# Kernel tuning notes

Hardware: AMD Instinct MI355X
Metric: run time of the kernel (lower is better)

Reference implementation:

```python
import jax, jax.numpy as jnp
import numpy as np

C = 512
HSIZE = C // 4
D, H, W = 18, 24, 24
N = D * H * W


def setup_inputs() -> dict:
    key = jax.random.key(0)
    ks = jax.random.split(key, 6)
    features = jax.random.normal(ks[0], (1, C, D, H, W), dtype=jnp.float32)
    Wi = jax.random.normal(ks[1], (HSIZE, C), dtype=jnp.float32) * 0.02
    bi = jax.random.normal(ks[2], (HSIZE,), dtype=jnp.float32) * 0.02
    Wj = jax.random.normal(ks[3], (HSIZE, C), dtype=jnp.float32) * 0.02
    bj = jax.random.normal(ks[4], (HSIZE,), dtype=jnp.float32) * 0.02
    # attention_agregate: shape (head=1, 1), xavier-uniform in the original
    agg = jax.random.uniform(ks[5], (1, 1), dtype=jnp.float32, minval=-1.0, maxval=1.0)
    return {"features": features, "Wi": Wi, "bi": bi, "Wj": Wj, "bj": bj, "agg": agg}


def reference(features, Wi, bi, Wj, bj, agg):
    # features: [1, C, D, H, W]; 1x1x1 convs == channel-wise matmuls
    x = features.reshape(C, N)                      # [C, N]
    fi = (Wi @ x + bi[:, None]).T                   # [N, hsize]  (conv_i output, permuted)
    fj = Wj @ x + bj[:, None]                       # [hsize, N]  (conv_j output)
    fk = x.T                                        # [N, C]      (raw features, NOT conv_k)
    # original: attn = (fi @ fj) * agg / N ; out = attn @ fk
    # linear chain reassociated: fi @ (fj @ fk) * agg / N  (same math, no NxN intermediate)
    scale = agg[0, 0] / jnp.float32(N)
    out_flat = (fi @ (fj @ fk)) * scale             # [N, C]
    return features + out_flat.T.reshape(1, C, D, H, W)
```

## Files before the change

### kernel.cpp

```cpp
#include <hip/hip_runtime.h>
#include <hip/hip_bf16.h>

#define C_   512
#define HS   128
#define NN   10368

typedef __bf16 bf16x8 __attribute__((ext_vector_type(8)));
typedef __bf16 bf16x2 __attribute__((ext_vector_type(2)));
typedef float  f32x4  __attribute__((ext_vector_type(4)));

__device__ __forceinline__ bf16x8 load_f32x8_as_bf16(const float* __restrict__ p) {
    float4 v0 = *(const float4*)p;
    float4 v1 = *(const float4*)(p + 4);
    bf16x8 o;
    o[0] = (__bf16)v0.x; o[1] = (__bf16)v0.y; o[2] = (__bf16)v0.z; o[3] = (__bf16)v0.w;
    o[4] = (__bf16)v1.x; o[5] = (__bf16)v1.y; o[6] = (__bf16)v1.z; o[7] = (__bf16)v1.w;
    return o;
}

__global__ void k_fused12(const float* __restrict__ feat,
                          const float* __restrict__ Wi, const float* __restrict__ Wj,
                          const float* __restrict__ bi, const float* __restrict__ bj,
                          __bf16* __restrict__ xb, __bf16* __restrict__ fj,
                          __bf16* __restrict__ finm, float* __restrict__ Mtf) {
    const int b = blockIdx.x;
    const int t = threadIdx.x;
    if (b >= 324) {
        const int j = b - 324;
        f32x4 z = {0.f, 0.f, 0.f, 0.f};
        float* p = Mtf + j * 4096 + t * 16;
        *(f32x4*)(p) = z; *(f32x4*)(p + 4) = z;
        *(f32x4*)(p + 8) = z; *(f32x4*)(p + 12) = z;
        return;
    }
    __shared__ __bf16 xt[32][520];
    const int n0 = b * 32;
    {
        const int tn = t & 31;
        const int c2 = (t >> 5) * 2;
        for (int cc = 0; cc < 512; cc += 16) {
            const int c = cc + c2;
            float v0 = feat[(size_t)c * NN + n0 + tn];
            float v1 = feat[(size_t)(c + 1) * NN + n0 + tn];
            __bf16 b0 = (__bf16)v0, b1 = (__bf16)v1;
            xb[(size_t)c * NN + n0 + tn]       = b0;
            xb[(size_t)(c + 1) * NN + n0 + tn] = b1;
            bf16x2 pk; pk[0] = b0; pk[1] = b1;
            *(bf16x2*)&xt[tn][c] = pk;
        }
    }
    __syncthreads();
    const int w    = t >> 6;
    const int lane = t & 63;
    const int l16  = lane & 15;
    const int q    = lane >> 4;
    const int h0   = w * 32;
    f32x4 afj[2][2] = {};
    f32x4 afi[2][2] = {};
    for (int k = 0; k < 512; k += 32) {
        bf16x8 ln[2], wj[2], wi[2];
        #pragma unroll
        for (int i = 0; i < 2; i++)
            ln[i] = *(const bf16x8*)&xt[16 * i + l16][k + q * 8];
        #pragma unroll
        for (int i = 0; i < 2; i++)
            wj[i] = load_f32x8_as_bf16(Wj + (h0 + 16 * i + l16) * 512 + k + q * 8);
        #pragma unroll
        for (int i = 0; i < 2; i++)
            wi[i] = load_f32x8_as_bf16(Wi + (h0 + 16 * i + l16) * 512 + k + q * 8);
        #pragma unroll
        for (int i = 0; i < 2; i++)
            #pragma unroll
            for (int tt = 0; tt < 2; tt++) {
                afj[i][tt] = __builtin_amdgcn_mfma_f32_16x16x32_bf16(wj[i], ln[tt], afj[i][tt], 0, 0, 0);
                afi[i][tt] = __builtin_amdgcn_mfma_f32_16x16x32_bf16(ln[i], wi[tt], afi[i][tt], 0, 0, 0);
            }
    }
    #pragma unroll
    for (int i = 0; i < 2; i++)
        #pragma unroll
        for (int tt = 0; tt < 2; tt++)
            #pragma unroll
            for (int r = 0; r < 4; r++) {
                {
                    int h = h0 + 16 * i + q * 4 + r;
                    int n = n0 + 16 * tt + l16;
                    fj[(size_t)h * NN + n] = (__bf16)(afj[i][tt][r] + bj[h]);
                }
                {
                    int n = n0 + 16 * i + q * 4 + r;
                    int h = h0 + 16 * tt + l16;
                    finm[(size_t)n * HS + h] = (__bf16)(afi[i][tt][r] + bi[h]);
                }
            }
}

__global__ void k_gemm3(const __bf16* __restrict__ xb, const __bf16* __restrict__ fj,
                        float* __restrict__ Mtf) {
    __shared__ float red[4][64][17];
    const int b    = blockIdx.x;
    const int t    = threadIdx.x;
    const int v    = t >> 6;
    const int lane = t & 63;
    const int l16  = lane & 15;
    const int q    = lane >> 4;
    const int tile = b & 63, g = b >> 6;
    const int c0 = (tile >> 2) * 32, h0 = (tile & 3) * 32;
    const int chunk = g * 4 + v;
    const int s0 = (chunk * 324) >> 5;
    const int s1 = ((chunk + 1) * 324) >> 5;
    f32x4 acc[2][2] = {};
    for (int s = s0; s < s1; s++) {
        int k = s * 32;
        bf16x8 a[2], bb[2];
        #pragma unroll
        for (int i = 0; i < 2; i++)
            a[i] = *(const bf16x8*)(xb + (size_t)(c0 + 16 * i + l16) * NN + k + q * 8);
        #pragma unroll
        for (int tt = 0; tt < 2; tt++)
            bb[tt] = *(const bf16x8*)(fj + (size_t)(h0 + 16 * tt + l16) * NN + k + q * 8);
        #pragma unroll
        for (int i = 0; i < 2; i++)
            #pragma unroll
            for (int tt = 0; tt < 2; tt++)
                acc[i][tt] = __builtin_amdgcn_mfma_f32_16x16x32_bf16(a[i], bb[tt], acc[i][tt], 0, 0, 0);
    }
    #pragma unroll
    for (int i = 0; i < 2; i++)
        #pragma unroll
        for (int tt = 0; tt < 2; tt++)
            #pragma unroll
            for (int r = 0; r < 4; r++)
                red[v][lane][i * 8 + tt * 4 + r] = acc[i][tt][r];
    __syncthreads();
    #pragma unroll
    for (int u = 0; u < 4; u++) {
        const int idx = t * 4 + u;
        const int lane_e = idx >> 4, j = idx & 15;
        float s = red[0][lane_e][j] + red[1][lane_e][j]
                + red[2][lane_e][j] + red[3][lane_e][j];
        const int i = j >> 3, tt = (j >> 2) & 1, r = j & 3;
        const int qe = lane_e >> 4, le = lane_e & 15;
        const int c = c0 + 16 * i + qe * 4 + r;
        const int h = h0 + 16 * tt + le;
        atomicAdd(&Mtf[c * HS + h], s);
    }
}

__global__ void k_gemm4(const float* __restrict__ Mtf, const __bf16* __restrict__ finm,
                        const float* __restrict__ feat, const float* __restrict__ agg,
                        float* __restrict__ out) {
    const int w    = blockIdx.x * 4 + (threadIdx.x >> 6);
    const int lane = threadIdx.x & 63;
    const int l16  = lane & 15;
    const int q    = lane >> 4;
    const int c0 = (w & 15) * 32, n0 = (w >> 4) * 64;
    const float scale = agg[0] * (1.0f / (float)NN);
    f32x4 acc[2][4] = {};
    for (int k = 0; k < 128; k += 32) {
        bf16x8 a[2], b[4];
        #pragma unroll
        for (int i = 0; i < 2; i++)
            a[i] = load_f32x8_as_bf16(Mtf + (c0 + 16 * i + l16) * HS + k + q * 8);
        #pragma unroll
        for (int tt = 0; tt < 4; tt++)
            b[tt] = *(const bf16x8*)(finm + (size_t)(n0 + 16 * tt + l16) * HS + k + q * 8);
        #pragma unroll
        for (int i = 0; i < 2; i++)
            #pragma unroll
            for (int tt = 0; tt < 4; tt++)
                acc[i][tt] = __builtin_amdgcn_mfma_f32_16x16x32_bf16(a[i], b[tt], acc[i][tt], 0, 0, 0);
    }
    #pragma unroll
    for (int i = 0; i < 2; i++)
        #pragma unroll
        for (int tt = 0; tt < 4; tt++)
            #pragma unroll
            for (int r = 0; r < 4; r++) {
                int c = c0 + 16 * i + q * 4 + r;
                int n = n0 + 16 * tt + l16;
                size_t idx = (size_t)c * NN + n;
                out[idx] = feat[idx] + scale * acc[i][tt][r];
            }
}

extern "C" void kernel_launch(void* const* d_in, const int* in_sizes, int n_in,
                              void* d_out, int out_size, void* d_ws, size_t ws_size,
                              hipStream_t stream) {
    const float* feat = (const float*)d_in[0];
    const float* Wi   = (const float*)d_in[1];
    const float* bi   = (const float*)d_in[2];
    const float* Wj   = (const float*)d_in[3];
    const float* bj   = (const float*)d_in[4];
    const float* agg  = (const float*)d_in[5];
    float* out = (float*)d_out;

    char* ws = (char*)d_ws;
    __bf16* xb   = (__bf16*)(ws);
    __bf16* fj   = (__bf16*)(ws + 10616832);
    __bf16* finm = (__bf16*)(ws + 13271040);
    float*  Mtf  = (float*) (ws + 15925248);

    k_fused12<<<340, 256, 0, stream>>>(feat, Wi, Wj, bi, bj, xb, fj, finm, Mtf);
    k_gemm3<<<512, 256, 0, stream>>>(xb, fj, Mtf);
    k_gemm4<<<648, 256, 0, stream>>>(Mtf, finm, feat, agg, out);
}
```

Before: 137.5 us.

## Split fused projection into staging and GEMM kernels, raise grid parallelism

```diff
diff --git a/kernel.cpp b/kernel.cpp
--- a/kernel.cpp
+++ b/kernel.cpp
@@ -6,6 +6,7 @@
 #define NN   10368
 
 typedef __bf16 bf16x8 __attribute__((ext_vector_type(8)));
+typedef __bf16 bf16x4 __attribute__((ext_vector_type(4)));
 typedef __bf16 bf16x2 __attribute__((ext_vector_type(2)));
 typedef float  f32x4  __attribute__((ext_vector_type(4)));
 
@@ -18,86 +19,118 @@
     return o;
 }
 
-__global__ void k_fused12(const float* __restrict__ feat,
-                          const float* __restrict__ Wi, const float* __restrict__ Wj,
-                          const float* __restrict__ bi, const float* __restrict__ bj,
-                          __bf16* __restrict__ xb, __bf16* __restrict__ fj,
-                          __bf16* __restrict__ finm, float* __restrict__ Mtf) {
+__global__ void k_stage(const float* __restrict__ feat,
+                        const float* __restrict__ Wi, const float* __restrict__ Wj,
+                        __bf16* __restrict__ xb, __bf16* __restrict__ xt,
+                        __bf16* __restrict__ Wib, __bf16* __restrict__ Wjb,
+                        float* __restrict__ Mtf) {
     const int b = blockIdx.x;
     const int t = threadIdx.x;
-    if (b >= 324) {
-        const int j = b - 324;
-        f32x4 z = {0.f, 0.f, 0.f, 0.f};
-        float* p = Mtf + j * 4096 + t * 16;
-        *(f32x4*)(p) = z; *(f32x4*)(p + 4) = z;
-        *(f32x4*)(p + 8) = z; *(f32x4*)(p + 12) = z;
+    if (b >= 1296) {
+        const int j = b - 1296;
+        if (j < 4) {
+            const float* src = (j < 2) ? Wj : Wi;
+            __bf16* dst = (j < 2) ? Wjb : Wib;
+            const int off = (j & 1) * 32768;
+            #pragma unroll 4
+            for (int u = 0; u < 32; u++) {
+                const int idx = off + u * 1024 + t * 4;
+                float4 v = *(const float4*)(src + idx);
+                bf16x4 o;
+                o[0] = (__bf16)v.x; o[1] = (__bf16)v.y;
+                o[2] = (__bf16)v.z; o[3] = (__bf16)v.w;
+                *(bf16x4*)(dst + idx) = o;
+            }
+        } else {
+            const int z = j - 4;
+            f32x4 zv = {0.f, 0.f, 0.f, 0.f};
+            float* p = Mtf + z * 4096 + t * 16;
+            *(f32x4*)(p) = zv; *(f32x4*)(p + 4) = zv;
+            *(f32x4*)(p + 8) = zv; *(f32x4*)(p + 12) = zv;
+        }
         return;
     }
-    __shared__ __bf16 xt[32][520];
-    const int n0 = b * 32;
-    {
-        const int tn = t & 31;
-        const int c2 = (t >> 5) * 2;
-        for (int cc = 0; cc < 512; cc += 16) {
-            const int c = cc + c2;
-            float v0 = feat[(size_t)c * NN + n0 + tn];
-            float v1 = feat[(size_t)(c + 1) * NN + n0 + tn];
-            __bf16 b0 = (__bf16)v0, b1 = (__bf16)v1;
-            xb[(size_t)c * NN + n0 + tn]       = b0;
-            xb[(size_t)(c + 1) * NN + n0 + tn] = b1;
-            bf16x2 pk; pk[0] = b0; pk[1] = b1;
-            *(bf16x2*)&xt[tn][c] = pk;
+    __shared__ __bf16 ldt[64][66];
+    const int bn = b >> 3, bc = b & 7;
+    const int n0 = bn * 64, c0 = bc * 64;
+    const int i = t & 15;
+    const int g = t >> 4;
+    const int nl = 4 * i;
+    #pragma unroll
+    for (int p = 0; p < 2; p++) {
+        const int cl = 2 * g + 32 * p;
+        const float* s = feat + (size_t)(c0 + cl) * NN + n0 + nl;
+        float4 v0 = *(const float4*)s;
+        float4 v1 = *(const float4*)(s + NN);
+        bf16x4 o0, o1;
+        o0[0] = (__bf16)v0.x; o0[1] = (__bf16)v0.y; o0[2] = (__bf16)v0.z; o0[3] = (__bf16)v0.w;
+        o1[0] = (__bf16)v1.x; o1[1] = (__bf16)v1.y; o1[2] = (__bf16)v1.z; o1[3] = (__bf16)v1.w;
+        *(bf16x4*)(xb + (size_t)(c0 + cl) * NN + n0 + nl)     = o0;
+        *(bf16x4*)(xb + (size_t)(c0 + cl + 1) * NN + n0 + nl) = o1;
+        #pragma unroll
+        for (int jj = 0; jj < 4; jj++) {
+            bf16x2 pk; pk[0] = o0[jj]; pk[1] = o1[jj];
+            *(bf16x2*)&ldt[nl + jj][cl] = pk;
         }
     }
     __syncthreads();
-    const int w    = t >> 6;
+    #pragma unroll
+    for (int p = 0; p < 4; p++) {
+        const int nr = g + 16 * p;
+        const int cw = 4 * i;
+        bf16x2 a0 = *(const bf16x2*)&ldt[nr][cw];
+        bf16x2 a1 = *(const bf16x2*)&ldt[nr][cw + 2];
+        bf16x4 o; o[0] = a0[0]; o[1] = a0[1]; o[2] = a1[0]; o[3] = a1[1];
+        *(bf16x4*)(xt + (size_t)(n0 + nr) * C_ + c0 + cw) = o;
+    }
+}
+
+__global__ void k_gemm12(const __bf16* __restrict__ xt,
+                         const __bf16* __restrict__ Wjb, const __bf16* __restrict__ Wib,
+                         const float* __restrict__ bi, const float* __restrict__ bj,
+                         __bf16* __restrict__ fj, __bf16* __restrict__ finm) {
+    const int b = blockIdx.x;
+    const int t = threadIdx.x;
+    const int w = t >> 6;
     const int lane = t & 63;
-    const int l16  = lane & 15;
-    const int q    = lane >> 4;
-    const int h0   = w * 32;
-    f32x4 afj[2][2] = {};
-    f32x4 afi[2][2] = {};
+    const int l16 = lane & 15;
+    const int q   = lane >> 4;
+    const int n0 = (b >> 1) * 32;
+    const int h0 = (b & 1) * 64 + w * 16;
+    f32x4 afj[2] = {};
+    f32x4 afi[2] = {};
+    #pragma unroll 4
     for (int k = 0; k < 512; k += 32) {
-        bf16x8 ln[2], wj[2], wi[2];
-        #pragma unroll
-        for (int i = 0; i < 2; i++)
-            ln[i] = *(const bf16x8*)&xt[16 * i + l16][k + q * 8];
-        #pragma unroll
-        for (int i = 0; i < 2; i++)
-            wj[i] = load_f32x8_as_bf16(Wj + (h0 + 16 * i + l16) * 512 + k + q * 8);
-        #pragma unroll
-        for (int i = 0; i < 2; i++)
-            wi[i] = load_f32x8_as_bf16(Wi + (h0 + 16 * i + l16) * 512 + k + q * 8);
-        #pragma unroll
-        for (int i = 0; i < 2; i++)
-            #pragma unroll
-            for (int tt = 0; tt < 2; tt++) {
-                afj[i][tt] = __builtin_amdgcn_mfma_f32_16x16x32_bf16(wj[i], ln[tt], afj[i][tt], 0, 0, 0);
-                afi[i][tt] = __builtin_amdgcn_mfma_f32_16x16x32_bf16(ln[i], wi[tt], afi[i][tt], 0, 0, 0);
-            }
-    }
-    #pragma unroll
-    for (int i = 0; i < 2; i++)
-        #pragma unroll
-        for (int tt = 0; tt < 2; tt++)
-            #pragma unroll
-            for (int r = 0; r < 4; r++) {
-                {
-                    int h = h0 + 16 * i + q * 4 + r;
-                    int n = n0 + 16 * tt + l16;
-                    fj[(size_t)h * NN + n] = (__bf16)(afj[i][tt][r] + bj[h]);
-                }
-                {
-                    int n = n0 + 16 * i + q * 4 + r;
-                    int h = h0 + 16 * tt + l16;
-                    finm[(size_t)n * HS + h] = (__bf16)(afi[i][tt][r] + bi[h]);
-                }
-            }
+        bf16x8 ln0 = *(const bf16x8*)&xt[(size_t)(n0 + l16) * C_ + k + q * 8];
+        bf16x8 ln1 = *(const bf16x8*)&xt[(size_t)(n0 + 16 + l16) * C_ + k + q * 8];
+        bf16x8 wjf = *(const bf16x8*)&Wjb[(size_t)(h0 + l16) * C_ + k + q * 8];
+        bf16x8 wif = *(const bf16x8*)&Wib[(size_t)(h0 + l16) * C_ + k + q * 8];
+        afj[0] = __builtin_amdgcn_mfma_f32_16x16x32_bf16(wjf, ln0, afj[0], 0, 0, 0);
+        afj[1] = __builtin_amdgcn_mfma_f32_16x16x32_bf16(wjf, ln1, afj[1], 0, 0, 0);
+        afi[0] = __builtin_amdgcn_mfma_f32_16x16x32_bf16(ln0, wif, afi[0], 0, 0, 0);
+        afi[1] = __builtin_amdgcn_mfma_f32_16x16x32_bf16(ln1, wif, afi[1], 0, 0, 0);
+    }
+    #pragma unroll
+    for (int tt = 0; tt < 2; tt++)
+        #pragma unroll
+        for (int r = 0; r < 4; r++) {
+            const int h = h0 + q * 4 + r;
+            const int n = n0 + 16 * tt + l16;
+            fj[(size_t)h * NN + n] = (__bf16)(afj[tt][r] + bj[h]);
+        }
+    #pragma unroll
+    for (int i2 = 0; i2 < 2; i2++)
+        #pragma unroll
+        for (int r = 0; r < 4; r++) {
+            const int n = n0 + 16 * i2 + q * 4 + r;
+            const int h = h0 + l16;
+            finm[(size_t)n * HS + h] = (__bf16)(afi[i2][r] + bi[h]);
+        }
 }
 
 __global__ void k_gemm3(const __bf16* __restrict__ xb, const __bf16* __restrict__ fj,
                         float* __restrict__ Mtf) {
-    __shared__ float red[4][64][17];
+    __shared__ float red[8][64][17];
     const int b    = blockIdx.x;
     const int t    = threadIdx.x;
     const int v    = t >> 6;
@@ -106,12 +139,13 @@
     const int q    = lane >> 4;
     const int tile = b & 63, g = b >> 6;
     const int c0 = (tile >> 2) * 32, h0 = (tile & 3) * 32;
-    const int chunk = g * 4 + v;
-    const int s0 = (chunk * 324) >> 5;
-    const int s1 = ((chunk + 1) * 324) >> 5;
+    const int chunk = g * 8 + v;
+    const int s0 = (chunk * 324) >> 6;
+    const int s1 = ((chunk + 1) * 324) >> 6;
     f32x4 acc[2][2] = {};
+    #pragma unroll 2
     for (int s = s0; s < s1; s++) {
-        int k = s * 32;
+        const int k = s * 32;
         bf16x8 a[2], bb[2];
         #pragma unroll
         for (int i = 0; i < 2; i++)
@@ -134,11 +168,12 @@
                 red[v][lane][i * 8 + tt * 4 + r] = acc[i][tt][r];
     __syncthreads();
     #pragma unroll
-    for (int u = 0; u < 4; u++) {
-        const int idx = t * 4 + u;
+    for (int u = 0; u < 2; u++) {
+        const int idx = t * 2 + u;
         const int lane_e = idx >> 4, j = idx & 15;
-        float s = red[0][lane_e][j] + red[1][lane_e][j]
-                + red[2][lane_e][j] + red[3][lane_e][j];
+        float s = 0.f;
+        #pragma unroll
+        for (int vv = 0; vv < 8; vv++) s += red[vv][lane_e][j];
         const int i = j >> 3, tt = (j >> 2) & 1, r = j & 3;
         const int qe = lane_e >> 4, le = lane_e & 15;
         const int c = c0 + 16 * i + qe * 4 + r;
@@ -154,32 +189,33 @@
     const int lane = threadIdx.x & 63;
     const int l16  = lane & 15;
     const int q    = lane >> 4;
-    const int c0 = (w & 15) * 32, n0 = (w >> 4) * 64;
+    const int c0 = (w & 15) * 32, n0 = (w >> 4) * 32;
     const float scale = agg[0] * (1.0f / (float)NN);
-    f32x4 acc[2][4] = {};
+    f32x4 acc[2][2] = {};
+    #pragma unroll
     for (int k = 0; k < 128; k += 32) {
-        bf16x8 a[2], b[4];
+        bf16x8 a[2], b[2];
         #pragma unroll
         for (int i = 0; i < 2; i++)
             a[i] = load_f32x8_as_bf16(Mtf + (c0 + 16 * i + l16) * HS + k + q * 8);
         #pragma unroll
-        for (int tt = 0; tt < 4; tt++)
+        for (int tt = 0; tt < 2; tt++)
             b[tt] = *(const bf16x8*)(finm + (size_t)(n0 + 16 * tt + l16) * HS + k + q * 8);
         #pragma unroll
         for (int i = 0; i < 2; i++)
             #pragma unroll
-            for (int tt = 0; tt < 4; tt++)
+            for (int tt = 0; tt < 2; tt++)
                 acc[i][tt] = __builtin_amdgcn_mfma_f32_16x16x32_bf16(a[i], b[tt], acc[i][tt], 0, 0, 0);
     }
     #pragma unroll
     for (int i = 0; i < 2; i++)
         #pragma unroll
-        for (int tt = 0; tt < 4; tt++)
+        for (int tt = 0; tt < 2; tt++)
             #pragma unroll
             for (int r = 0; r < 4; r++) {
-                int c = c0 + 16 * i + q * 4 + r;
-                int n = n0 + 16 * tt + l16;
-                size_t idx = (size_t)c * NN + n;
+                const int c = c0 + 16 * i + q * 4 + r;
+                const int n = n0 + 16 * tt + l16;
+                const size_t idx = (size_t)c * NN + n;
                 out[idx] = feat[idx] + scale * acc[i][tt][r];
             }
 }
@@ -200,8 +236,12 @@
     __bf16* fj   = (__bf16*)(ws + 10616832);
     __bf16* finm = (__bf16*)(ws + 13271040);
     float*  Mtf  = (float*) (ws + 15925248);
-
-    k_fused12<<<340, 256, 0, stream>>>(feat, Wi, Wj, bi, bj, xb, fj, finm, Mtf);
-    k_gemm3<<<512, 256, 0, stream>>>(xb, fj, Mtf);
-    k_gemm4<<<648, 256, 0, stream>>>(Mtf, finm, feat, agg, out);
-}
+    __bf16* xt   = (__bf16*)(ws + 16187392);
+    __bf16* Wjb  = (__bf16*)(ws + 26804224);
+    __bf16* Wib  = (__bf16*)(ws + 26935296);
+
+    k_stage <<<1316, 256, 0, stream>>>(feat, Wi, Wj, xb, xt, Wib, Wjb, Mtf);
+    k_gemm12<<<648,  256, 0, stream>>>(xt, Wjb, Wib, bi, bj, fj, finm);
+    k_gemm3 <<<512,  512, 0, stream>>>(xb, fj, Mtf);
+    k_gemm4 <<<1296, 256, 0, stream>>>(Mtf, finm, feat, agg, out);
+}
```

After: 142.7 us. +3.8%, slower.

## Double threads per block, split K across more waves, prefetch loads

Applied to the files above, without the earlier changes.

```diff
diff --git a/kernel.cpp b/kernel.cpp
--- a/kernel.cpp
+++ b/kernel.cpp
@@ -18,19 +18,19 @@
     return o;
 }
 
-__global__ void k_fused12(const float* __restrict__ feat,
-                          const float* __restrict__ Wi, const float* __restrict__ Wj,
-                          const float* __restrict__ bi, const float* __restrict__ bj,
-                          __bf16* __restrict__ xb, __bf16* __restrict__ fj,
-                          __bf16* __restrict__ finm, float* __restrict__ Mtf) {
+__global__ __launch_bounds__(512, 2)
+void k_fused12(const float* __restrict__ feat,
+               const float* __restrict__ Wi, const float* __restrict__ Wj,
+               const float* __restrict__ bi, const float* __restrict__ bj,
+               __bf16* __restrict__ xb, __bf16* __restrict__ fj,
+               __bf16* __restrict__ finm, float* __restrict__ Mtf) {
     const int b = blockIdx.x;
     const int t = threadIdx.x;
     if (b >= 324) {
-        const int j = b - 324;
-        f32x4 z = {0.f, 0.f, 0.f, 0.f};
-        float* p = Mtf + j * 4096 + t * 16;
-        *(f32x4*)(p) = z; *(f32x4*)(p + 4) = z;
-        *(f32x4*)(p + 8) = z; *(f32x4*)(p + 12) = z;
+        const int z = b - 324;
+        f32x4 zv = {0.f, 0.f, 0.f, 0.f};
+        float* p = Mtf + z * 4096 + t * 8;
+        *(f32x4*)(p) = zv; *(f32x4*)(p + 4) = zv;
         return;
     }
     __shared__ __bf16 xt[32][520];
@@ -38,11 +38,17 @@
     {
         const int tn = t & 31;
         const int c2 = (t >> 5) * 2;
-        for (int cc = 0; cc < 512; cc += 16) {
-            const int c = cc + c2;
-            float v0 = feat[(size_t)c * NN + n0 + tn];
-            float v1 = feat[(size_t)(c + 1) * NN + n0 + tn];
-            __bf16 b0 = (__bf16)v0, b1 = (__bf16)v1;
+        float va[16], vb[16];
+        #pragma unroll
+        for (int p = 0; p < 16; p++) {
+            const int c = p * 32 + c2;
+            va[p] = feat[(size_t)c * NN + n0 + tn];
+            vb[p] = feat[(size_t)(c + 1) * NN + n0 + tn];
+        }
+        #pragma unroll
+        for (int p = 0; p < 16; p++) {
+            const int c = p * 32 + c2;
+            __bf16 b0 = (__bf16)va[p], b1 = (__bf16)vb[p];
             xb[(size_t)c * NN + n0 + tn]       = b0;
             xb[(size_t)(c + 1) * NN + n0 + tn] = b1;
             bf16x2 pk; pk[0] = b0; pk[1] = b1;
@@ -54,50 +60,44 @@
     const int lane = t & 63;
     const int l16  = lane & 15;
     const int q    = lane >> 4;
-    const int h0   = w * 32;
-    f32x4 afj[2][2] = {};
-    f32x4 afi[2][2] = {};
+    const int h0   = w * 16;
+    f32x4 afj[2] = {};
+    f32x4 afi[2] = {};
+    #pragma unroll 4
     for (int k = 0; k < 512; k += 32) {
-        bf16x8 ln[2], wj[2], wi[2];
-        #pragma unroll
-        for (int i = 0; i < 2; i++)
-            ln[i] = *(const bf16x8*)&xt[16 * i + l16][k + q * 8];
-        #pragma unroll
-        for (int i = 0; i < 2; i++)
-            wj[i] = load_f32x8_as_bf16(Wj + (h0 + 16 * i + l16) * 512 + k + q * 8);
-        #pragma unroll
-        for (int i = 0; i < 2; i++)
-            wi[i] = load_f32x8_as_bf16(Wi + (h0 + 16 * i + l16) * 512 + k + q * 8);
-        #pragma unroll
-        for (int i = 0; i < 2; i++)
-            #pragma unroll
-            for (int tt = 0; tt < 2; tt++) {
-                afj[i][tt] = __builtin_amdgcn_mfma_f32_16x16x32_bf16(wj[i], ln[tt], afj[i][tt], 0, 0, 0);
-                afi[i][tt] = __builtin_amdgcn_mfma_f32_16x16x32_bf16(ln[i], wi[tt], afi[i][tt], 0, 0, 0);
-            }
-    }
-    #pragma unroll
-    for (int i = 0; i < 2; i++)
-        #pragma unroll
-        for (int tt = 0; tt < 2; tt++)
-            #pragma unroll
-            for (int r = 0; r < 4; r++) {
-                {
-                    int h = h0 + 16 * i + q * 4 + r;
-                    int n = n0 + 16 * tt + l16;
-                    fj[(size_t)h * NN + n] = (__bf16)(afj[i][tt][r] + bj[h]);
-                }
-                {
-                    int n = n0 + 16 * i + q * 4 + r;
-                    int h = h0 + 16 * tt + l16;
-                    finm[(size_t)n * HS + h] = (__bf16)(afi[i][tt][r] + bi[h]);
-                }
-            }
-}
-
-__global__ void k_gemm3(const __bf16* __restrict__ xb, const __bf16* __restrict__ fj,
-                        float* __restrict__ Mtf) {
-    __shared__ float red[4][64][17];
+        bf16x8 ln0 = *(const bf16x8*)&xt[l16][k + q * 8];
+        bf16x8 ln1 = *(const bf16x8*)&xt[16 + l16][k + q * 8];
+        bf16x8 wjf = load_f32x8_as_bf16(Wj + (h0 + l16) * 512 + k + q * 8);
+        bf16x8 wif = load_f32x8_as_bf16(Wi + (h0 + l16) * 512 + k + q * 8);
+        afj[0] = __builtin_amdgcn_mfma_f32_16x16x32_bf16(wjf, ln0, afj[0], 0, 0, 0);
+        afj[1] = __builtin_amdgcn_mfma_f32_16x16x32_bf16(wjf, ln1, afj[1], 0, 0, 0);
+        afi[0] = __builtin_amdgcn_mfma_f32_16x16x32_bf16(ln0, wif, afi[0], 0, 0, 0);
+        afi[1] = __builtin_amdgcn_mfma_f32_16x16x32_bf16(ln1, wif, afi[1], 0, 0, 0);
+    }
+    const float4 bjv = *(const float4*)(bj + h0 + q * 4);
+    const float  biv = bi[h0 + l16];
+    #pragma unroll
+    for (int tt = 0; tt < 2; tt++)
+        #pragma unroll
+        for (int r = 0; r < 4; r++) {
+            const int h = h0 + q * 4 + r;
+            const int n = n0 + 16 * tt + l16;
+            fj[(size_t)h * NN + n] = (__bf16)(afj[tt][r] + (&bjv.x)[r]);
+        }
+    #pragma unroll
+    for (int i2 = 0; i2 < 2; i2++)
+        #pragma unroll
+        for (int r = 0; r < 4; r++) {
+            const int n = n0 + 16 * i2 + q * 4 + r;
+            const int h = h0 + l16;
+            finm[(size_t)n * HS + h] = (__bf16)(afi[i2][r] + biv);
+        }
+}
+
+__global__ __launch_bounds__(512, 2)
+void k_gemm3(const __bf16* __restrict__ xb, const __bf16* __restrict__ fj,
+             float* __restrict__ Mtf) {
+    __shared__ float red[8][64][17];
     const int b    = blockIdx.x;
     const int t    = threadIdx.x;
     const int v    = t >> 6;
@@ -106,25 +106,37 @@
     const int q    = lane >> 4;
     const int tile = b & 63, g = b >> 6;
     const int c0 = (tile >> 2) * 32, h0 = (tile & 3) * 32;
-    const int chunk = g * 4 + v;
-    const int s0 = (chunk * 324) >> 5;
-    const int s1 = ((chunk + 1) * 324) >> 5;
+    const int chunk = g * 8 + v;
+    const int s0 = (chunk * 324) >> 6;
+    const int s1 = ((chunk + 1) * 324) >> 6;
     f32x4 acc[2][2] = {};
-    for (int s = s0; s < s1; s++) {
-        int k = s * 32;
-        bf16x8 a[2], bb[2];
-        #pragma unroll
-        for (int i = 0; i < 2; i++)
-            a[i] = *(const bf16x8*)(xb + (size_t)(c0 + 16 * i + l16) * NN + k + q * 8);
-        #pragma unroll
-        for (int tt = 0; tt < 2; tt++)
-            bb[tt] = *(const bf16x8*)(fj + (size_t)(h0 + 16 * tt + l16) * NN + k + q * 8);
+    bf16x8 a[2], bb[2];
+    {
+        const int k = s0 * 32;
+        a[0]  = *(const bf16x8*)(xb + (size_t)(c0 + l16) * NN + k + q * 8);
+        a[1]  = *(const bf16x8*)(xb + (size_t)(c0 + 16 + l16) * NN + k + q * 8);
+        bb[0] = *(const bf16x8*)(fj + (size_t)(h0 + l16) * NN + k + q * 8);
+        bb[1] = *(const bf16x8*)(fj + (size_t)(h0 + 16 + l16) * NN + k + q * 8);
+    }
+    for (int s = s0; s < s1 - 1; s++) {
+        const int kn = (s + 1) * 32;
+        bf16x8 a2[2], b2[2];
+        a2[0] = *(const bf16x8*)(xb + (size_t)(c0 + l16) * NN + kn + q * 8);
+        a2[1] = *(const bf16x8*)(xb + (size_t)(c0 + 16 + l16) * NN + kn + q * 8);
+        b2[0] = *(const bf16x8*)(fj + (size_t)(h0 + l16) * NN + kn + q * 8);
+        b2[1] = *(const bf16x8*)(fj + (size_t)(h0 + 16 + l16) * NN + kn + q * 8);
         #pragma unroll
         for (int i = 0; i < 2; i++)
             #pragma unroll
             for (int tt = 0; tt < 2; tt++)
                 acc[i][tt] = __builtin_amdgcn_mfma_f32_16x16x32_bf16(a[i], bb[tt], acc[i][tt], 0, 0, 0);
-    }
+        a[0] = a2[0]; a[1] = a2[1]; bb[0] = b2[0]; bb[1] = b2[1];
+    }
+    #pragma unroll
+    for (int i = 0; i < 2; i++)
+        #pragma unroll
+        for (int tt = 0; tt < 2; tt++)
+            acc[i][tt] = __builtin_amdgcn_mfma_f32_16x16x32_bf16(a[i], bb[tt], acc[i][tt], 0, 0, 0);
     #pragma unroll
     for (int i = 0; i < 2; i++)
         #pragma unroll
@@ -134,11 +146,12 @@
                 red[v][lane][i * 8 + tt * 4 + r] = acc[i][tt][r];
     __syncthreads();
     #pragma unroll
-    for (int u = 0; u < 4; u++) {
-        const int idx = t * 4 + u;
+    for (int u = 0; u < 2; u++) {
+        const int idx = t * 2 + u;
         const int lane_e = idx >> 4, j = idx & 15;
-        float s = red[0][lane_e][j] + red[1][lane_e][j]
-                + red[2][lane_e][j] + red[3][lane_e][j];
+        float s = 0.f;
+        #pragma unroll
+        for (int vv = 0; vv < 8; vv++) s += red[vv][lane_e][j];
         const int i = j >> 3, tt = (j >> 2) & 1, r = j & 3;
         const int qe = lane_e >> 4, le = lane_e & 15;
         const int c = c0 + 16 * i + qe * 4 + r;
@@ -147,40 +160,52 @@
     }
 }
 
-__global__ void k_gemm4(const float* __restrict__ Mtf, const __bf16* __restrict__ finm,
-                        const float* __restrict__ feat, const float* __restrict__ agg,
-                        float* __restrict__ out) {
+__global__ __launch_bounds__(256, 2)
+void k_gemm4(const float* __restrict__ Mtf, const __bf16* __restrict__ finm,
+             const float* __restrict__ feat, const float* __restrict__ agg,
+             float* __restrict__ out) {
     const int w    = blockIdx.x * 4 + (threadIdx.x >> 6);
     const int lane = threadIdx.x & 63;
     const int l16  = lane & 15;
     const int q    = lane >> 4;
-    const int c0 = (w & 15) * 32, n0 = (w >> 4) * 64;
+    const int c0 = (w & 15) * 32, n0 = (w >> 4) * 32;
     const float scale = agg[0] * (1.0f / (float)NN);
-    f32x4 acc[2][4] = {};
+    f32x4 acc[2][2] = {};
+    #pragma unroll
     for (int k = 0; k < 128; k += 32) {
-        bf16x8 a[2], b[4];
+        bf16x8 a[2], b[2];
         #pragma unroll
         for (int i = 0; i < 2; i++)
             a[i] = load_f32x8_as_bf16(Mtf + (c0 + 16 * i + l16) * HS + k + q * 8);
         #pragma unroll
-        for (int tt = 0; tt < 4; tt++)
+        for (int tt = 0; tt < 2; tt++)
             b[tt] = *(const bf16x8*)(finm + (size_t)(n0 + 16 * tt + l16) * HS + k + q * 8);
         #pragma unroll
         for (int i = 0; i < 2; i++)
             #pragma unroll
-            for (int tt = 0; tt < 4; tt++)
+            for (int tt = 0; tt < 2; tt++)
                 acc[i][tt] = __builtin_amdgcn_mfma_f32_16x16x32_bf16(a[i], b[tt], acc[i][tt], 0, 0, 0);
     }
-    #pragma unroll
-    for (int i = 0; i < 2; i++)
-        #pragma unroll
-        for (int tt = 0; tt < 4; tt++)
+    float fv[2][2][4];
+    #pragma unroll
+    for (int i = 0; i < 2; i++)
+        #pragma unroll
+        for (int tt = 0; tt < 2; tt++)
             #pragma unroll
             for (int r = 0; r < 4; r++) {
-                int c = c0 + 16 * i + q * 4 + r;
-                int n = n0 + 16 * tt + l16;
-                size_t idx = (size_t)c * NN + n;
-                out[idx] = feat[idx] + scale * acc[i][tt][r];
+                const int c = c0 + 16 * i + q * 4 + r;
+                const int n = n0 + 16 * tt + l16;
+                fv[i][tt][r] = feat[(size_t)c * NN + n];
+            }
+    #pragma unroll
+    for (int i = 0; i < 2; i++)
+        #pragma unroll
+        for (int tt = 0; tt < 2; tt++)
+            #pragma unroll
+            for (int r = 0; r < 4; r++) {
+                const int c = c0 + 16 * i + q * 4 + r;
+                const int n = n0 + 16 * tt + l16;
+                out[(size_t)c * NN + n] = fv[i][tt][r] + scale * acc[i][tt][r];
             }
 }
 
@@ -201,7 +226,7 @@
     __bf16* finm = (__bf16*)(ws + 13271040);
     float*  Mtf  = (float*) (ws + 15925248);
 
-    k_fused12<<<340, 256, 0, stream>>>(feat, Wi, Wj, bi, bj, xb, fj, finm, Mtf);
-    k_gemm3<<<512, 256, 0, stream>>>(xb, fj, Mtf);
-    k_gemm4<<<648, 256, 0, stream>>>(Mtf, finm, feat, agg, out);
-}
+    k_fused12<<<340,  512, 0, stream>>>(feat, Wi, Wj, bi, bj, xb, fj, finm, Mtf);
+    k_gemm3 <<<512,  512, 0, stream>>>(xb, fj, Mtf);
+    k_gemm4 <<<1296, 256, 0, stream>>>(Mtf, finm, feat, agg, out);
+}
```

Result: slower. 142.3 us (+3.6%).
